# Performance work log

Hardware: AMD Instinct MI355X
Metric: run time of the kernel (lower is better)

Reference implementation:

```python
import jax, jax.numpy as jnp
import numpy as np

N = 50000   # nodes
R = 3       # relations
E = 300000  # edges per relation
H, D = 4, 32  # heads, per-head dim (hidden_feat=128)
IN, HID, OUT = 128, 128, 64
SLOPE = 0.2  # DGL GATConv leaky_relu negative slope


def setup_inputs() -> dict:
    key = jax.random.key(0)
    ks = jax.random.split(key, 12)
    s = 0.05
    return {
        "x": jax.random.normal(ks[0], (N, IN), jnp.float32),
        "edges": jax.random.randint(ks[1], (R, 2, E), 0, N, jnp.int64),
        "W1": jax.random.normal(ks[2], (R, IN, H * D), jnp.float32) * s,
        "al1": jax.random.normal(ks[3], (R, H, D), jnp.float32) * s,
        "ar1": jax.random.normal(ks[4], (R, H, D), jnp.float32) * s,
        "b1": jnp.zeros((R, H, D), jnp.float32),
        "W2": jax.random.normal(ks[5], (R, HID, H * D), jnp.float32) * s,
        "al2": jax.random.normal(ks[6], (R, H, D), jnp.float32) * s,
        "ar2": jax.random.normal(ks[7], (R, H, D), jnp.float32) * s,
        "b2": jnp.zeros((R, H, D), jnp.float32),
        "Wl": jax.random.normal(ks[8], (HID, OUT), jnp.float32) * s,
        "bl": jnp.zeros((OUT,), jnp.float32),
    }


def rgat_layer(h, edges, W, al, ar, b):
    """HeteroGraphConv(sum) of per-relation GATConv. h: [N,F]. Returns [N,H,D]."""
    out = jnp.zeros((N, H, D), h.dtype)
    for r in range(R):  # small fixed relation count
        src, dst = edges[r, 0], edges[r, 1]
        feat = (h @ W[r]).reshape(N, H, D)                  # per-relation projection
        el = jnp.einsum("nhd,hd->nh", feat, al[r])          # [N,H]
        er = jnp.einsum("nhd,hd->nh", feat, ar[r])          # [N,H]
        e = jax.nn.leaky_relu(el[src] + er[dst], SLOPE)      # [E,H]
        # edge softmax over incoming edges per destination node
        emax = jax.ops.segment_max(e, dst, num_segments=N)   # [N,H]
        ex = jnp.exp(e - emax[dst])
        denom = jax.ops.segment_sum(ex, dst, num_segments=N) # [N,H]
        alpha = ex / denom[dst]                               # [E,H]
        msg = feat[src] * alpha[:, :, None]                   # [E,H,D]
        out = out + jax.ops.segment_sum(msg, dst, num_segments=N) + b[r]
    return out


def reference(x, edges, W1, al1, ar1, b1, W2, al2, ar2, b2, Wl, bl):
    h = rgat_layer(x, edges, W1, al1, ar1, b1).reshape(N, H * D)
    h = jax.nn.relu(h)  # dropout is identity in eval mode
    h = rgat_layer(h, edges, W2, al2, ar2, b2).reshape(N, H * D)
    return h @ Wl + bl  # [N, OUT]
```

## Files before the change

kernel.cpp:

```cpp
#include <hip/hip_runtime.h>
#include <hip/hip_bf16.h>
#include <hip/hip_fp16.h>
#include <type_traits>

#define Nn 50000
#define RR 3
#define EE 300000

typedef __attribute__((ext_vector_type(8))) short short8;
typedef __attribute__((ext_vector_type(4))) short short4v;
typedef __attribute__((ext_vector_type(4))) float floatx4;

__device__ __forceinline__ short f2bf(float f) {
    __hip_bfloat16 h = __float2bfloat16(f);
    return *reinterpret_cast<short*>(&h);
}
__device__ __forceinline__ float bf2f(short s) {
    __hip_bfloat16 h = *reinterpret_cast<__hip_bfloat16*>(&s);
    return __bfloat162float(h);
}


__global__ void init_kernel(const float* __restrict__ W1, const float* __restrict__ W2,
                            short* __restrict__ Z, int* __restrict__ counts,
                            int* __restrict__ totals) {
    int bx = blockIdx.x;
    if (bx < 586) {
        int i = bx * 256 + threadIdx.x;
        if (i < RR * Nn) counts[i] = 0;
        if (i < 4) totals[i] = 0;
    } else {
        int idx = (bx - 586) * 256 + threadIdx.x;
        if (idx >= 12288) return;
        int lane = idx & 63;
        int nt = (idx >> 6) & 7;
        int kt = (idx >> 9) & 3;
        int rl = idx >> 11;
        int layer = rl / 3, r = rl % 3;
        const float* W = (layer ? W2 : W1) + (size_t)r * 16384;
        int n = nt * 16 + (lane & 15);
        int k0 = kt * 32 + (lane >> 4) * 8;
        short8 v;
        #pragma unroll
        for (int j = 0; j < 8; ++j) v[j] = f2bf(W[(size_t)(k0 + j) * 128 + n]);
        *(short8*)&Z[(size_t)idx * 8] = v;
    }
}


__global__ void count_kernel(const int* __restrict__ edges, int* __restrict__ counts,
                             int* __restrict__ ord) {
    int i = blockIdx.x * blockDim.x + threadIdx.x;
    if (i >= RR * EE / 8) return;
    int g = i * 8;
    int r = g / EE, e0 = g - r * EE;
    const int* db = &edges[(size_t)r * 2 * EE + EE + e0];
    int4 d0 = *(const int4*)db;
    int4 d1 = *(const int4*)(db + 4);
    int* cb = counts + r * Nn;
    int4 o0, o1;
    o0.x = atomicAdd(&cb[d0.x], 1);
    o0.y = atomicAdd(&cb[d0.y], 1);
    o0.z = atomicAdd(&cb[d0.z], 1);
    o0.w = atomicAdd(&cb[d0.w], 1);
    o1.x = atomicAdd(&cb[d1.x], 1);
    o1.y = atomicAdd(&cb[d1.y], 1);
    o1.z = atomicAdd(&cb[d1.z], 1);
    o1.w = atomicAdd(&cb[d1.w], 1);
    *(int4*)&ord[g] = o0;
    *(int4*)&ord[g + 4] = o1;
}

__global__ __launch_bounds__(256) void alloc_kernel(const int* __restrict__ counts,
                                                    int* __restrict__ row_start,
                                                    int* __restrict__ totals) {
    __shared__ int s[256];
    __shared__ int base_s;
    int r = blockIdx.y;
    int tid = threadIdx.x;
    int n = blockIdx.x * 256 + tid;
    int idx = r * Nn + n;
    int c = (n < Nn) ? counts[idx] : 0;
    s[tid] = c;
    __syncthreads();
    #pragma unroll
    for (int off = 1; off < 256; off <<= 1) {
        int v = 0;
        if (tid >= off) v = s[tid - off];
        __syncthreads();
        if (tid >= off) s[tid] += v;
        __syncthreads();
    }
    if (tid == 255) base_s = atomicAdd(&totals[r], s[255]);
    __syncthreads();
    if (n < Nn) row_start[idx] = base_s + s[tid] - c;
}

__global__ void scatter_kernel(const int* __restrict__ edges, const int* __restrict__ ord,
                               const int* __restrict__ row_start,
                               int* __restrict__ csr_s, int* __restrict__ csr_d) {
    int i = blockIdx.x * blockDim.x + threadIdx.x;
    if (i >= RR * EE / 8) return;
    int g = i * 8;
    int r = g / EE, e0 = g - r * EE;
    const int* sb = &edges[(size_t)r * 2 * EE + e0];
    const int* db = sb + EE;
    int4 s0 = *(const int4*)sb, s1 = *(const int4*)(sb + 4);
    int4 d0 = *(const int4*)db, d1 = *(const int4*)(db + 4);
    int4 o0 = *(const int4*)&ord[g], o1 = *(const int4*)&ord[g + 4];
    const int* rs = row_start + r * Nn;
    int* cs = csr_s + (size_t)r * EE;
    int* cd = csr_d + (size_t)r * EE;
    int p0 = rs[d0.x] + o0.x, p1 = rs[d0.y] + o0.y;
    int p2 = rs[d0.z] + o0.z, p3 = rs[d0.w] + o0.w;
    int p4 = rs[d1.x] + o1.x, p5 = rs[d1.y] + o1.y;
    int p6 = rs[d1.z] + o1.z, p7 = rs[d1.w] + o1.w;
    cs[p0] = s0.x; cs[p1] = s0.y; cs[p2] = s0.z; cs[p3] = s0.w;
    cs[p4] = s1.x; cs[p5] = s1.y; cs[p6] = s1.z; cs[p7] = s1.w;
    cd[p0] = d0.x; cd[p1] = d0.y; cd[p2] = d0.z; cd[p3] = d0.w;
    cd[p4] = d1.x; cd[p5] = d1.y; cd[p6] = d1.z; cd[p7] = d1.w;
}


template<typename TA>
__global__ __launch_bounds__(256) void gemm_proj_mfma(const TA* __restrict__ A,
                                                      const short* __restrict__ Z,
                                                      const float* __restrict__ al,
                                                      const float* __restrict__ ar,
                                                      __half* __restrict__ C,
                                                      float* __restrict__ el,
                                                      float* __restrict__ er) {
    __shared__ short A_lds[64 * 136];
    __shared__ float al_lds[384], ar_lds[384];
    int tid = threadIdx.x;
    int row0 = blockIdx.x * 64;
    if (tid < 128) { al_lds[256 + tid] = al[256 + tid]; ar_lds[256 + tid] = ar[256 + tid]; }
    al_lds[tid] = al[tid]; ar_lds[tid] = ar[tid];
    if constexpr (std::is_same<TA, float>::value) {
        #pragma unroll
        for (int p = 0; p < 8; ++p) {
            int f = p * 256 + tid;
            int row = f >> 5;
            int c4 = (f & 31) * 4;
            float4 v = make_float4(0.f, 0.f, 0.f, 0.f);
            if (row0 + row < Nn) v = *(const float4*)&A[(size_t)(row0 + row) * 128 + c4];
            short4v sv;
            sv[0] = f2bf(v.x); sv[1] = f2bf(v.y); sv[2] = f2bf(v.z); sv[3] = f2bf(v.w);
            *(short4v*)&A_lds[row * 136 + c4] = sv;
        }
    } else {
        #pragma unroll
        for (int p = 0; p < 4; ++p) {
            int c = p * 256 + tid;
            int row = c >> 4, c8 = (c & 15) * 8;
            short8 v = (short8)(0);
            if (row0 + row < Nn) v = *(const short8*)&A[(size_t)(row0 + row) * 128 + c8];
            *(short8*)&A_lds[row * 136 + c8] = v;
        }
    }
    __syncthreads();
    int wave = tid >> 6, lane = tid & 63;
    int m = lane & 15, q = lane >> 4;
    short8 af[4];
    #pragma unroll
    for (int kt = 0; kt < 4; ++kt)
        af[kt] = *(short8*)&A_lds[(wave * 16 + m) * 136 + kt * 32 + q * 8];
    __syncthreads();
    __half* lds_h = (__half*)A_lds;
    int row8 = tid >> 2;
    int hh = tid & 3;
    for (int r = 0; r < RR; ++r) {
        floatx4 acc[8];
        #pragma unroll
        for (int nt = 0; nt < 8; ++nt) acc[nt] = (floatx4)(0.f);
        const short* Zr = Z + (size_t)r * 16384;
        #pragma unroll
        for (int kt = 0; kt < 4; ++kt) {
            #pragma unroll
            for (int nt = 0; nt < 8; ++nt) {
                short8 bf = *(const short8*)&Zr[(size_t)(kt * 8 + nt) * 512 + lane * 8];
                acc[nt] = __builtin_amdgcn_mfma_f32_16x16x32_bf16(af[kt], bf, acc[nt], 0, 0, 0);
            }
        }
        #pragma unroll
        for (int nt = 0; nt < 8; ++nt) {
            int col = nt * 16 + m;
            #pragma unroll
            for (int reg = 0; reg < 4; ++reg)
                lds_h[(wave * 16 + q * 4 + reg) * 136 + col] = __float2half(acc[nt][reg]);
        }
        __syncthreads();
        __half* Cr = C + (size_t)r * Nn * 128;
        #pragma unroll
        for (int p = 0; p < 4; ++p) {
            int lin = p * 256 + tid;
            int row = lin >> 4, c8 = (lin & 15) * 8;
            if (row0 + row < Nn)
                *(short8*)&Cr[(size_t)(row0 + row) * 128 + c8] = *(short8*)&lds_h[row * 136 + c8];
        }
        {
            const __half2* fp = (const __half2*)&lds_h[row8 * 136 + hh * 32];
            const float* alp = &al_lds[r * 128 + hh * 32];
            const float* arp = &ar_lds[r * 128 + hh * 32];
            float sl = 0.f, sr = 0.f;
            #pragma unroll
            for (int d = 0; d < 16; ++d) {
                float2 v = __half22float2(fp[d]);
                sl += v.x * alp[2 * d] + v.y * alp[2 * d + 1];
                sr += v.x * arp[2 * d] + v.y * arp[2 * d + 1];
            }
            if (row0 + row8 < Nn) {
                size_t ei = (size_t)(r * Nn + row0 + row8) * 4 + hh;
                el[ei] = sl;
                er[ei] = sr;
            }
        }
        __syncthreads();
    }
}


__global__ __launch_bounds__(256) void gemm_final_kernel(const float* __restrict__ A,
                                                         const float* __restrict__ Wl,
                                                         const float* __restrict__ bl,
                                                         float* __restrict__ out) {
    __shared__ float As[16][65];
    __shared__ float Bs[16][65];
    int tid = threadIdx.x;
    int row0 = blockIdx.x * 64;
    float acc[4][4] = {};
    int tx = tid & 15, ty = tid >> 4;
    for (int k0 = 0; k0 < 128; k0 += 16) {
        {
            int mm = tid >> 2, c = (tid & 3) * 4;
            int row = row0 + mm;
            float4 v = make_float4(0.f, 0.f, 0.f, 0.f);
            if (row < Nn) v = *(const float4*)&A[(size_t)row * 128 + k0 + c];
            As[c + 0][mm] = v.x; As[c + 1][mm] = v.y; As[c + 2][mm] = v.z; As[c + 3][mm] = v.w;
        }
        {
            int kk = tid >> 4, j = (tid & 15) * 4;
            float4 v = *(const float4*)&Wl[(size_t)(k0 + kk) * 64 + j];
            *(float4*)&Bs[kk][j] = v;
        }
        __syncthreads();
        #pragma unroll
        for (int kk = 0; kk < 16; ++kk) {
            float4 a = *(const float4*)&As[kk][ty * 4];
            float4 b = *(const float4*)&Bs[kk][tx * 4];
            float av[4] = {a.x, a.y, a.z, a.w};
            float bv[4] = {b.x, b.y, b.z, b.w};
            #pragma unroll
            for (int i = 0; i < 4; ++i)
                #pragma unroll
                for (int j = 0; j < 4; ++j) acc[i][j] += av[i] * bv[j];
        }
        __syncthreads();
    }
    float4 bias = *(const float4*)&bl[tx * 4];
    #pragma unroll
    for (int i = 0; i < 4; ++i) {
        int row = row0 + ty * 4 + i;
        if (row >= Nn) continue;
        float4 v = make_float4(acc[i][0] + bias.x, acc[i][1] + bias.y,
                               acc[i][2] + bias.z, acc[i][3] + bias.w);
        *(float4*)&out[(size_t)row * 64 + tx * 4] = v;
    }
}


__global__ __launch_bounds__(256) void wexp_kernel(const int* __restrict__ csr_s,
                                                   const int* __restrict__ csr_d,
                                                   const float* __restrict__ el,
                                                   const float* __restrict__ er,
                                                   __half* __restrict__ wq) {
    int r = blockIdx.y;
    int k = blockIdx.x * 256 + threadIdx.x;
    if (k >= EE) return;
    size_t gk = (size_t)r * EE + k;
    int es = csr_s[gk], ed = csr_d[gk];
    float4 l4 = *(const float4*)&el[(size_t)(r * Nn + es) * 4];
    float4 r4 = *(const float4*)&er[(size_t)(r * Nn + ed) * 4];
    float lv[4] = {l4.x, l4.y, l4.z, l4.w};
    float rv[4] = {r4.x, r4.y, r4.z, r4.w};
    #pragma unroll
    for (int h = 0; h < 4; ++h) {
        float x = lv[h] + rv[h];
        x = (x > 0.f) ? x : 0.2f * x;
        wq[(size_t)h * (RR * EE) + gk] = __float2half(__expf(x));
    }
}


template<bool OUT_BF16_RELU>
__global__ __launch_bounds__(256) void agg_kernel(const __half2* __restrict__ feat2,
                                                  const __half* __restrict__ wq,
                                                  const int* __restrict__ csr_s,
                                                  const int* __restrict__ row_start,
                                                  const int* __restrict__ counts,
                                                  const float* __restrict__ b,
                                                  void* __restrict__ out) {
    int wave = threadIdx.x >> 6;
    int lane = threadIdx.x & 63;
    int n = blockIdx.x * 4 + wave;
    if (n >= Nn) return;
    int h = lane >> 4;
    int hl = lane & 15;
    int grp = lane & 48;
    int t2 = lane * 2;
    int cntA[RR], stA[RR], sC[RR];
    float wC[RR];
    #pragma unroll
    for (int r = 0; r < RR; ++r) {
        cntA[r] = counts[r * Nn + n];
        stA[r] = row_start[r * Nn + n];
    }
    #pragma unroll
    for (int r = 0; r < RR; ++r) {
        sC[r] = 0; wC[r] = 0.f;
        if (hl < cntA[r]) {
            int idx = stA[r] + hl;
            sC[r] = csr_s[(size_t)r * EE + idx];
            wC[r] = __half2float(wq[(size_t)h * (RR * EE) + (size_t)r * EE + idx]);
        }
    }
    float accx = b[t2] + b[128 + t2] + b[256 + t2];
    float accy = b[t2 + 1] + b[128 + t2 + 1] + b[256 + t2 + 1];
    #pragma unroll
    for (int r = 0; r < RR; ++r) {
        int cnt = cntA[r];
        if (cnt == 0) continue;
        const __half2* fr = feat2 + (size_t)r * Nn * 64;
        float den = 0.f, numx = 0.f, numy = 0.f;
        int s_l = sC[r];
        float w_l = wC[r];
        int i0 = 0;
        while (true) {
            int mm = cnt - i0; if (mm > 16) mm = 16;
            int mm8 = (mm + 7) & ~7;
            for (int j = 0; j < mm8; j += 8) {
                int s0 = __shfl(s_l, j);
                int s1 = __shfl(s_l, j + 1);
                int s2 = __shfl(s_l, j + 2);
                int s3 = __shfl(s_l, j + 3);
                int s4 = __shfl(s_l, j + 4);
                int s5 = __shfl(s_l, j + 5);
                int s6 = __shfl(s_l, j + 6);
                int s7 = __shfl(s_l, j + 7);
                float w0 = __shfl(w_l, grp | j);
                float w1 = __shfl(w_l, grp | (j + 1));
                float w2 = __shfl(w_l, grp | (j + 2));
                float w3 = __shfl(w_l, grp | (j + 3));
                float w4 = __shfl(w_l, grp | (j + 4));
                float w5 = __shfl(w_l, grp | (j + 5));
                float w6 = __shfl(w_l, grp | (j + 6));
                float w7 = __shfl(w_l, grp | (j + 7));
                __half2 f0 = fr[(size_t)s0 * 64 + lane];
                __half2 f1 = fr[(size_t)s1 * 64 + lane];
                __half2 f2 = fr[(size_t)s2 * 64 + lane];
                __half2 f3 = fr[(size_t)s3 * 64 + lane];
                __half2 f4 = fr[(size_t)s4 * 64 + lane];
                __half2 f5 = fr[(size_t)s5 * 64 + lane];
                __half2 f6 = fr[(size_t)s6 * 64 + lane];
                __half2 f7 = fr[(size_t)s7 * 64 + lane];
                float2 g0 = __half22float2(f0), g1 = __half22float2(f1);
                float2 g2 = __half22float2(f2), g3 = __half22float2(f3);
                float2 g4 = __half22float2(f4), g5 = __half22float2(f5);
                float2 g6 = __half22float2(f6), g7 = __half22float2(f7);
                den += ((w0 + w1) + (w2 + w3)) + ((w4 + w5) + (w6 + w7));
                numx += (w0 * g0.x + w1 * g1.x + w2 * g2.x + w3 * g3.x)
                      + (w4 * g4.x + w5 * g5.x + w6 * g6.x + w7 * g7.x);
                numy += (w0 * g0.y + w1 * g1.y + w2 * g2.y + w3 * g3.y)
                      + (w4 * g4.y + w5 * g5.y + w6 * g6.y + w7 * g7.y);
            }
            i0 += 16;
            if (i0 >= cnt) break;
            s_l = 0; w_l = 0.f;
            if (i0 + hl < cnt) {
                int idx = stA[r] + i0 + hl;
                s_l = csr_s[(size_t)r * EE + idx];
                w_l = __half2float(wq[(size_t)h * (RR * EE) + (size_t)r * EE + idx]);
            }
        }
        float inv = 1.f / den;
        accx += numx * inv;
        accy += numy * inv;
    }
    if constexpr (OUT_BF16_RELU) {
        short* o = (short*)out;
        short2 pk;
        pk.x = f2bf(fmaxf(accx, 0.f));
        pk.y = f2bf(fmaxf(accy, 0.f));
        *(short2*)&o[(size_t)n * 128 + t2] = pk;
    } else {
        float* o = (float*)out;
        *(float2*)&o[(size_t)n * 128 + t2] = make_float2(accx, accy);
    }
}


extern "C" void kernel_launch(void* const* d_in, const int* in_sizes, int n_in,
                              void* d_out, int out_size, void* d_ws, size_t ws_size,
                              hipStream_t stream) {
    const float* x   = (const float*)d_in[0];
    const int*  edges = (const int*)d_in[1];
    const float* W1  = (const float*)d_in[2];
    const float* al1 = (const float*)d_in[3];
    const float* ar1 = (const float*)d_in[4];
    const float* b1  = (const float*)d_in[5];
    const float* W2  = (const float*)d_in[6];
    const float* al2 = (const float*)d_in[7];
    const float* ar2 = (const float*)d_in[8];
    const float* b2  = (const float*)d_in[9];
    const float* Wl  = (const float*)d_in[10];
    const float* bl  = (const float*)d_in[11];
    float* out = (float*)d_out;

    __half* feat  = (__half*)d_ws;
    short* Z      = (short*)(feat + (size_t)RR * Nn * 128);
    float* el     = (float*)(Z + 98304);
    float* er     = el + (size_t)RR * Nn * 4;
    float* outbuf = er + (size_t)RR * Nn * 4;
    __half* wq    = (__half*)(outbuf + (size_t)Nn * 128);
    int* counts    = (int*)(wq + (size_t)4 * RR * EE);
    int* row_start = counts + RR * Nn;
    int* totals    = row_start + RR * Nn;
    int* ord       = totals + 4;
    int* csr_s     = ord + RR * EE;
    int* csr_d     = csr_s + RR * EE;
    short* outb16  = (short*)outbuf;

    const int rowBlocks  = (Nn + 63) / 64;
    const int nodeBlocks = (Nn + 255) / 256;
    const int aggBlocks  = (Nn + 3) / 4;
    const int edgeBlocks = (EE + 255) / 256;
    const int edge8Blocks = (RR * EE / 8 + 255) / 256;

    init_kernel<<<634, 256, 0, stream>>>(W1, W2, Z, counts, totals);
    count_kernel<<<edge8Blocks, 256, 0, stream>>>(edges, counts, ord);
    alloc_kernel<<<dim3(nodeBlocks, RR), 256, 0, stream>>>(counts, row_start, totals);
    scatter_kernel<<<edge8Blocks, 256, 0, stream>>>(edges, ord, row_start, csr_s, csr_d);

    gemm_proj_mfma<float><<<rowBlocks, 256, 0, stream>>>(x, Z, al1, ar1, feat, el, er);
    wexp_kernel<<<dim3(edgeBlocks, RR), 256, 0, stream>>>(csr_s, csr_d, el, er, wq);
    agg_kernel<true><<<aggBlocks, 256, 0, stream>>>((const __half2*)feat, wq, csr_s, row_start, counts, b1, outb16);

    gemm_proj_mfma<short><<<rowBlocks, 256, 0, stream>>>(outb16, Z + 49152, al2, ar2, feat, el, er);
    wexp_kernel<<<dim3(edgeBlocks, RR), 256, 0, stream>>>(csr_s, csr_d, el, er, wq);
    agg_kernel<false><<<aggBlocks, 256, 0, stream>>>((const __half2*)feat, wq, csr_s, row_start, counts, b2, outbuf);

    gemm_final_kernel<<<rowBlocks, 256, 0, stream>>>(outbuf, Wl, bl, out);
}
```

Measured before the change: 337.7 us.

## Fuse CSR scatter into first projection GEMM and weight swizzle into count

Replaces the init kernel with a hipMemsetAsync for counts and totals. The weight-swizzle blocks move into the count kernel as extra blocks, and the CSR scatter runs as extra blocks inside the first-layer projection GEMM launch. This removes two kernel launches and lets independent work share launches, so scatter can overlap with the MFMA GEMM. The buffer layout is reordered so counts and totals sit next to each other for a single memset. The cost is heterogeneous blocks in one grid, where the GEMM's LDS allocation may limit how many scatter blocks fit on a CU.

Result: no change. 331.9 us (-1.7%).

```diff
diff --git a/kernel.cpp b/kernel.cpp
--- a/kernel.cpp
+++ b/kernel.cpp
@@ -15,22 +15,15 @@
     __hip_bfloat16 h = __float2bfloat16(f);
     return *reinterpret_cast<short*>(&h);
 }
-__device__ __forceinline__ float bf2f(short s) {
-    __hip_bfloat16 h = *reinterpret_cast<__hip_bfloat16*>(&s);
-    return __bfloat162float(h);
-}
-
-
-__global__ void init_kernel(const float* __restrict__ W1, const float* __restrict__ W2,
-                            short* __restrict__ Z, int* __restrict__ counts,
-                            int* __restrict__ totals) {
+
+
+__global__ void count_wswz_kernel(const int* __restrict__ edges, int* __restrict__ counts,
+                                  int* __restrict__ ord,
+                                  const float* __restrict__ W1, const float* __restrict__ W2,
+                                  short* __restrict__ Z) {
     int bx = blockIdx.x;
-    if (bx < 586) {
-        int i = bx * 256 + threadIdx.x;
-        if (i < RR * Nn) counts[i] = 0;
-        if (i < 4) totals[i] = 0;
-    } else {
-        int idx = (bx - 586) * 256 + threadIdx.x;
+    if (bx >= 440) {
+        int idx = (bx - 440) * 256 + threadIdx.x;
         if (idx >= 12288) return;
         int lane = idx & 63;
         int nt = (idx >> 6) & 7;
@@ -44,13 +37,9 @@
         #pragma unroll
         for (int j = 0; j < 8; ++j) v[j] = f2bf(W[(size_t)(k0 + j) * 128 + n]);
         *(short8*)&Z[(size_t)idx * 8] = v;
-    }
-}
-
-
-__global__ void count_kernel(const int* __restrict__ edges, int* __restrict__ counts,
-                             int* __restrict__ ord) {
-    int i = blockIdx.x * blockDim.x + threadIdx.x;
+        return;
+    }
+    int i = bx * 256 + threadIdx.x;
     if (i >= RR * EE / 8) return;
     int g = i * 8;
     int r = g / EE, e0 = g - r * EE;
@@ -96,10 +85,12 @@
     if (n < Nn) row_start[idx] = base_s + s[tid] - c;
 }
 
-__global__ void scatter_kernel(const int* __restrict__ edges, const int* __restrict__ ord,
-                               const int* __restrict__ row_start,
-                               int* __restrict__ csr_s, int* __restrict__ csr_d) {
-    int i = blockIdx.x * blockDim.x + threadIdx.x;
+
+__device__ __forceinline__ void scatter_body(int bid, const int* __restrict__ edges,
+                                             const int* __restrict__ ord,
+                                             const int* __restrict__ row_start,
+                                             int* __restrict__ csr_s, int* __restrict__ csr_d) {
+    int i = bid * 256 + threadIdx.x;
     if (i >= RR * EE / 8) return;
     int g = i * 8;
     int r = g / EE, e0 = g - r * EE;
@@ -122,14 +113,24 @@
 }
 
 
-template<typename TA>
+template<typename TA, bool FUSE_SCATTER>
 __global__ __launch_bounds__(256) void gemm_proj_mfma(const TA* __restrict__ A,
                                                       const short* __restrict__ Z,
                                                       const float* __restrict__ al,
                                                       const float* __restrict__ ar,
                                                       __half* __restrict__ C,
                                                       float* __restrict__ el,
-                                                      float* __restrict__ er) {
+                                                      float* __restrict__ er,
+                                                      const int* __restrict__ edges,
+                                                      const int* __restrict__ ord,
+                                                      const int* __restrict__ row_start,
+                                                      int* __restrict__ csr_s,
+                                                      int* __restrict__ csr_d) {
+    const int rowBlocks = (Nn + 63) / 64;
+    if (FUSE_SCATTER && blockIdx.x >= rowBlocks) {
+        scatter_body(blockIdx.x - rowBlocks, edges, ord, row_start, csr_s, csr_d);
+        return;
+    }
     __shared__ short A_lds[64 * 136];
     __shared__ float al_lds[384], ar_lds[384];
     int tid = threadIdx.x;
@@ -423,9 +424,9 @@
     float* outbuf = er + (size_t)RR * Nn * 4;
     __half* wq    = (__half*)(outbuf + (size_t)Nn * 128);
     int* counts    = (int*)(wq + (size_t)4 * RR * EE);
-    int* row_start = counts + RR * Nn;
-    int* totals    = row_start + RR * Nn;
-    int* ord       = totals + 4;
+    int* totals    = counts + RR * Nn;
+    int* row_start = totals + 4;
+    int* ord       = row_start + RR * Nn;
     int* csr_s     = ord + RR * EE;
     int* csr_d     = csr_s + RR * EE;
     short* outb16  = (short*)outbuf;
@@ -436,16 +437,17 @@
     const int edgeBlocks = (EE + 255) / 256;
     const int edge8Blocks = (RR * EE / 8 + 255) / 256;
 
-    init_kernel<<<634, 256, 0, stream>>>(W1, W2, Z, counts, totals);
-    count_kernel<<<edge8Blocks, 256, 0, stream>>>(edges, counts, ord);
+    hipMemsetAsync(counts, 0, (size_t)(RR * Nn + 4) * sizeof(int), stream);
+    count_wswz_kernel<<<440 + 48, 256, 0, stream>>>(edges, counts, ord, W1, W2, Z);
     alloc_kernel<<<dim3(nodeBlocks, RR), 256, 0, stream>>>(counts, row_start, totals);
-    scatter_kernel<<<edge8Blocks, 256, 0, stream>>>(edges, ord, row_start, csr_s, csr_d);
-
-    gemm_proj_mfma<float><<<rowBlocks, 256, 0, stream>>>(x, Z, al1, ar1, feat, el, er);
+
+    gemm_proj_mfma<float, true><<<rowBlocks + edge8Blocks, 256, 0, stream>>>(
+        x, Z, al1, ar1, feat, el, er, edges, ord, row_start, csr_s, csr_d);
     wexp_kernel<<<dim3(edgeBlocks, RR), 256, 0, stream>>>(csr_s, csr_d, el, er, wq);
     agg_kernel<true><<<aggBlocks, 256, 0, stream>>>((const __half2*)feat, wq, csr_s, row_start, counts, b1, outb16);
 
-    gemm_proj_mfma<short><<<rowBlocks, 256, 0, stream>>>(outb16, Z + 49152, al2, ar2, feat, el, er);
+    gemm_proj_mfma<short, false><<<rowBlocks, 256, 0, stream>>>(
+        outb16, Z + 49152, al2, ar2, feat, el, er, nullptr, nullptr, nullptr, nullptr, nullptr);
     wexp_kernel<<<dim3(edgeBlocks, RR), 256, 0, stream>>>(csr_s, csr_d, el, er, wq);
     agg_kernel<false><<<aggBlocks, 256, 0, stream>>>((const __half2*)feat, wq, csr_s, row_start, counts, b2, outbuf);
 
```
